# Performance work log

Hardware: AMD Instinct MI355X
Metric: run time of the kernel (lower is better)

The kernel has to match this reference:

```python
import jax, jax.numpy as jnp
import numpy as np

N = 40000          # spots (nodes)
G = 3000           # genes (input features)
C = 20             # num_classes
E = N * 16         # edges (avg degree 16)


def _uniform(key, shape, stdv):
    return jax.random.uniform(key, shape, jnp.float32, -stdv, stdv)


def _linear_params(key, n_in, n_out):
    # torch Linear default init: U(-1/sqrt(in), 1/sqrt(in)); stored as [in, out]
    k1, k2 = jax.random.split(key)
    s = 1.0 / np.sqrt(n_in)
    return _uniform(k1, (n_in, n_out), s), _uniform(k2, (n_out,), s)


def setup_inputs() -> dict:
    key = jax.random.key(0)
    ks = jax.random.split(key, 32)
    x = jax.random.normal(ks[0], (N, G), jnp.float32)
    adj_rows = jax.random.randint(ks[1], (E,), 0, N, jnp.int32)
    adj_cols = jax.random.randint(ks[2], (E,), 0, N, jnp.int32)
    adj_vals = jax.random.uniform(ks[3], (E,), jnp.float32)

    # GCN weights: GraphConvolution init U(-1/sqrt(out), 1/sqrt(out)), no bias
    def gcn_w(k, fi, fo):
        return _uniform(k, (fi, fo), 1.0 / np.sqrt(fo))

    inp = {
        "x": x, "adj_rows": adj_rows, "adj_cols": adj_cols, "adj_vals": adj_vals,
        "W1": gcn_w(ks[4], G, 512), "W2": gcn_w(ks[5], 512, 256),
        "W3": gcn_w(ks[6], 256, 128), "W4": gcn_w(ks[7], 128, 128),
        "W5": gcn_w(ks[8], 128, C),
    }
    # AE linear layers
    for name, (fi, fo), k in [
        ("enc1", (G, 512), ks[9]), ("enc2", (512, 256), ks[10]),
        ("enc3", (256, 128), ks[11]), ("zl", (128, 128), ks[12]),
        ("dec1", (128, 128), ks[13]), ("dec2", (128, 256), ks[14]),
        ("dec3", (256, 512), ks[15]), ("xbar", (512, G), ks[16]),
    ]:
        w, b = _linear_params(k, fi, fo)
        inp[name + "_w"], inp[name + "_b"] = w, b
    # Attention projection vectors (Linear(in_size, 1, bias=False))
    inp["a1"] = _uniform(ks[17], (512,), 1.0 / np.sqrt(512))
    inp["a2"] = _uniform(ks[18], (256,), 1.0 / np.sqrt(256))
    inp["a3"] = _uniform(ks[19], (128,), 1.0 / np.sqrt(128))
    inp["a4"] = _uniform(ks[20], (128,), 1.0 / np.sqrt(128))
    inp["scale"] = jax.random.normal(ks[21], (G,), jnp.float32)
    inp["additive"] = jax.random.normal(ks[22], (G,), jnp.float32)
    return inp


def _spmm(rows, cols, vals, dense, n):
    # out[r] = sum_e vals[e] * dense[cols[e]] for rows[e]==r  (sparse [n,n] @ dense)
    return jax.ops.segment_sum(vals[:, None] * dense[cols], rows, num_segments=n)


def _gcn(x, rows, cols, vals, W, n, active=True):
    out = _spmm(rows, cols, vals, x @ W, n)
    return jax.nn.relu(out) if active else out


def _attn(h, t, a):
    # stack two [N,D] branches, softmax over the branch axis, weighted sum
    z = jnp.stack([h, t], axis=1)           # [N,2,D]
    w = jnp.einsum('nbd,d->nb', z, a)        # [N,2]
    beta = jax.nn.softmax(w, axis=1)
    return jnp.einsum('nb,nbd->nd', beta, z)


def reference(x, adj_rows, adj_cols, adj_vals,
              W1, W2, W3, W4, W5,
              enc1_w, enc1_b, enc2_w, enc2_b, enc3_w, enc3_b, zl_w, zl_b,
              dec1_w, dec1_b, dec2_w, dec2_b, dec3_w, dec3_b, xbar_w, xbar_b,
              a1, a2, a3, a4, scale, additive):
    n = x.shape[0]
    # autoencoder
    t1 = jax.nn.relu(x @ enc1_w + enc1_b)
    t2 = jax.nn.relu(t1 @ enc2_w + enc2_b)
    t3 = jax.nn.relu(t2 @ enc3_w + enc3_b)
    z = t3 @ zl_w + zl_b
    d1 = jax.nn.relu(z @ dec1_w + dec1_b)
    d2 = jax.nn.relu(d1 @ dec2_w + dec2_b)
    d3 = jax.nn.relu(d2 @ dec3_w + dec3_b)
    x_bar = d3 @ xbar_w + xbar_b
    # GCN stack with attention-fused AE skip connections
    h = _gcn(x, adj_rows, adj_cols, adj_vals, W1, n)
    emb = _attn(h, t1, a1)
    h = _gcn(emb, adj_rows, adj_cols, adj_vals, W2, n)
    emb = _attn(h, t2, a2)
    h = _gcn(emb, adj_rows, adj_cols, adj_vals, W3, n)
    emb = _attn(h, t3, a3)
    h = _gcn(emb, adj_rows, adj_cols, adj_vals, W4, n)
    emb = _attn(h, z, a4)
    output = _gcn(emb, adj_rows, adj_cols, adj_vals, W5, n, active=False)
    return output, x_bar, jax.nn.sigmoid(scale), jnp.exp(additive)
```

## Files before the change

### kernel.cpp

```cpp
#include <hip/hip_runtime.h>
#include <cmath>

typedef unsigned short u16;
typedef unsigned int u32;
typedef __attribute__((ext_vector_type(8))) short short8;
typedef __attribute__((ext_vector_type(4))) short short4v;
typedef __attribute__((ext_vector_type(4))) float f32x4;

__device__ __forceinline__ float bf2f(u16 h) {
  union { u32 u; float f; } v; v.u = ((u32)h) << 16; return v.f;
}
__device__ __forceinline__ u16 f2bf(float f) {
  union { float f; u32 u; } v; v.f = f;
  u32 u = v.u;
  u32 r = (u + 0x7FFFu + ((u >> 16) & 1u)) >> 16;
  return (u16)r;
}

__global__ void convx_kernel(const float* __restrict__ x, u16* __restrict__ A0) {
  int idx = blockIdx.x * 256 + threadIdx.x;
  int r = blockIdx.y;
  if (idx >= 752) return;
  short4v o;
  if (r < 40000 && idx < 750) {
    float4 v = *(const float4*)(x + (size_t)r * 3000 + idx * 4);
    o[0] = (short)f2bf(v.x); o[1] = (short)f2bf(v.y);
    o[2] = (short)f2bf(v.z); o[3] = (short)f2bf(v.w);
  } else {
    o[0] = 0; o[1] = 0; o[2] = 0; o[3] = 0;
  }
  *(short4v*)(A0 + (size_t)r * 3008 + idx * 4) = o;
}

__global__ void convw_kernel(const float* __restrict__ W, u16* __restrict__ Wt,
                             int K, int N, int Kp) {
  int k = blockIdx.x * 256 + threadIdx.x;
  int n = blockIdx.y;
  if (k >= Kp) return;
  float v = (k < K && n < N) ? W[(size_t)k * N + n] : 0.f;
  Wt[(size_t)n * Kp + k] = f2bf(v);
}

__global__ void zero_kernel(int* p, int n) {
  int i = blockIdx.x * 256 + threadIdx.x;
  if (i < n) p[i] = 0;
}
__global__ void count_kernel(const int* __restrict__ rows, int* __restrict__ counts, int E) {
  int i = blockIdx.x * 256 + threadIdx.x;
  if (i < E) atomicAdd(&counts[rows[i]], 1);
}
__global__ __launch_bounds__(1024) void scan_kernel(const int* __restrict__ counts,
                                                    int* __restrict__ rowptr,
                                                    int* __restrict__ cursor, int n) {
  __shared__ int buf[1024];
  __shared__ int carry_s;
  int tid = threadIdx.x;
  if (tid == 0) carry_s = 0;
  __syncthreads();
  for (int base = 0; base < n; base += 1024) {
    int i = base + tid;
    int v = (i < n) ? counts[i] : 0;
    buf[tid] = v;
    __syncthreads();
    for (int off = 1; off < 1024; off <<= 1) {
      int tv = (tid >= off) ? buf[tid - off] : 0;
      __syncthreads();
      buf[tid] += tv;
      __syncthreads();
    }
    int incl = buf[tid];
    int carry = carry_s;
    if (i < n) { int ex = carry + incl - v; rowptr[i] = ex; cursor[i] = ex; }
    __syncthreads();
    if (tid == 1023) carry_s = carry + incl;
    __syncthreads();
  }
  if (tid == 0) rowptr[n] = carry_s;
}
__global__ void scatter_kernel(const int* __restrict__ rows, const int* __restrict__ cols,
                               const float* __restrict__ vals, int* __restrict__ cursor,
                               int* __restrict__ cols_s, float* __restrict__ vals_s, int E) {
  int i = blockIdx.x * 256 + threadIdx.x;
  if (i < E) {
    int r = rows[i];
    int p = atomicAdd(&cursor[r], 1);
    cols_s[p] = cols[i];
    vals_s[p] = vals[i];
  }
}

#define BM 128
#define BN 128
#define BK 32

template <bool BIAS, bool RELU, bool OUTBF16, int CH>
__global__ __launch_bounds__(256, 2) void gemm_bf16(
    const u16* __restrict__ A, int lda, const u16* __restrict__ Bt, int ldb,
    void* __restrict__ C1, int ldc,
    const float* __restrict__ bias, int M, int Nreal, int K, int MT, int NT) {
  __shared__ __align__(16) u16 As[2][BM * BK];
  __shared__ __align__(16) u16 Bs[2][BN * BK];
  const int lin = blockIdx.x;
  const int per = CH * NT;
  const int g = lin / per;
  const int r0 = lin - g * per;
  const int bx0 = g * CH;
  const int cw = min(CH, MT - bx0);
  const int bx = bx0 + r0 % cw;
  const int by = r0 / cw;

  const int tid = threadIdx.x;
  const int lane = tid & 63;
  const int wave = tid >> 6;
  const int mblk = bx * BM;
  const int nblk = by * BN;
  const int wm = (wave & 1) * 64;
  const int wn = (wave >> 1) * 64;
  const int ml = lane & 15;
  const int kg = lane >> 4;

  f32x4 acc[4][4];
#pragma unroll
  for (int i = 0; i < 4; ++i)
#pragma unroll
    for (int j = 0; j < 4; ++j) acc[i][j] = (f32x4)(0.f);

  const int nk = K / BK;
  const int sr = tid >> 2;
  const int sc = (tid & 3) * 8;
  const u16* gA0 = A + (size_t)(mblk + sr) * lda + sc;
  const u16* gA1 = A + (size_t)(mblk + sr + 64) * lda + sc;
  const u16* gB0 = Bt + (size_t)(nblk + sr) * ldb + sc;
  const u16* gB1 = Bt + (size_t)(nblk + sr + 64) * ldb + sc;

  auto stage = [&](int buf, int kt) {
    const int ko = kt * BK;
    u16* lA = &As[buf][0] + wave * 512;
    u16* lB = &Bs[buf][0] + wave * 512;
    __builtin_amdgcn_global_load_lds((const void*)(gA0 + ko), (void*)lA, 16, 0, 0);
    __builtin_amdgcn_global_load_lds((const void*)(gA1 + ko), (void*)(lA + 2048), 16, 0, 0);
    __builtin_amdgcn_global_load_lds((const void*)(gB0 + ko), (void*)lB, 16, 0, 0);
    __builtin_amdgcn_global_load_lds((const void*)(gB1 + ko), (void*)(lB + 2048), 16, 0, 0);
  };

  stage(0, 0);
  asm volatile("s_waitcnt vmcnt(0)" ::: "memory");
  __syncthreads();

  int cur = 0;
  for (int kt = 0; kt < nk; ++kt) {
    if (kt + 1 < nk) stage(cur ^ 1, kt + 1);
    short8 af[4], bfr[4];
#pragma unroll
    for (int i = 0; i < 4; ++i) {
      af[i] = *(const short8*)&As[cur][(wm + i * 16 + ml) * BK + kg * 8];
      bfr[i] = *(const short8*)&Bs[cur][(wn + i * 16 + ml) * BK + kg * 8];
    }
#pragma unroll
    for (int i = 0; i < 4; ++i)
#pragma unroll
      for (int j = 0; j < 4; ++j)
        acc[i][j] = __builtin_amdgcn_mfma_f32_16x16x32_bf16(af[i], bfr[j], acc[i][j], 0, 0, 0);
    asm volatile("s_waitcnt vmcnt(0)" ::: "memory");
    __syncthreads();
    cur ^= 1;
  }

#pragma unroll
  for (int i = 0; i < 4; ++i) {
    const int row0 = mblk + wm + i * 16 + kg * 4;
#pragma unroll
    for (int j = 0; j < 4; ++j) {
      const int col = nblk + wn + j * 16 + ml;
      if (col < Nreal) {
        float bv = BIAS ? bias[col] : 0.f;
#pragma unroll
        for (int r = 0; r < 4; ++r) {
          const int row = row0 + r;
          if (row < M) {
            float v = acc[i][j][r] + bv;
            if (RELU) v = fmaxf(v, 0.f);
            if (OUTBF16)
              ((u16*)C1)[(size_t)row * ldc + col] = f2bf(v);
            else
              ((float*)C1)[(size_t)row * ldc + col] = v;
          }
        }
      }
    }
  }
}

template <bool BIAS, bool RELU, bool OUTBF16, bool SPLIT>
__global__ __launch_bounds__(512, 1) void gemm256(
    const u16* __restrict__ A, int lda, const u16* __restrict__ Bt, int ldb,
    void* __restrict__ C1, void* __restrict__ C2, int ldc,
    const float* __restrict__ bias, int M, int Nreal, int K, int MT2, int NT) {
  __shared__ __align__(16) u16 lds[2][2][256 * 64];
  const int tid = threadIdx.x;
  const int lane = tid & 63;
  const int wave = tid >> 6;
  const int wm = wave >> 2;
  const int wn = wave & 3;
  const int ml = lane & 15;
  const int kg = lane >> 4;

  const int grp = blockIdx.x / (8 * NT);
  const int rr = blockIdx.x % (8 * NT);
  const int nb = min(8, MT2 - grp * 8);
  const int bx = grp * 8 + rr % nb;
  const int by = rr / nb;
  const int mblk = bx * 256;
  const int nblk = by * 256;

  f32x4 acc[8][4];
#pragma unroll
  for (int i = 0; i < 8; ++i)
#pragma unroll
    for (int j = 0; j < 4; ++j) acc[i][j] = (f32x4)(0.f);

  const int srow = tid >> 3;
  const int clog = (tid & 7) ^ (srow & 7);
  const size_t abase = (size_t)(mblk + srow) * lda + clog * 8;
  const size_t bbase = (size_t)(nblk + srow) * ldb + clog * 8;
  const int NKT = K / 64;

  auto stageA = [&](int d, int kt, int h) {
    u16* dst = &lds[d][0][0] + h * 4096 + wave * 512;
    const u16* src = A + abase + (size_t)h * 64 * lda + kt * 64;
    __builtin_amdgcn_global_load_lds((const void*)src, (void*)dst, 16, 0, 0);
  };
  auto stageB = [&](int d, int kt, int h) {
    u16* dst = &lds[d][1][0] + h * 4096 + wave * 512;
    const u16* src = Bt + bbase + (size_t)h * 64 * ldb + kt * 64;
    __builtin_amdgcn_global_load_lds((const void*)src, (void*)dst, 16, 0, 0);
  };
  auto stageAll = [&](int d, int kt) {
    stageB(d, kt, 0); stageB(d, kt, 1); stageB(d, kt, 2); stageB(d, kt, 3);
    stageA(d, kt, 0); stageA(d, kt, 2); stageA(d, kt, 1); stageA(d, kt, 3);
  };
  auto readA = [&](int d, int im, int kk) -> short8 {
    const int r = wm * 128 + im * 16 + ml;
    const int ch = (kk * 4 + kg) ^ (r & 7);
    return *(const short8*)&lds[d][0][r * 64 + ch * 8];
  };
  auto readB = [&](int d, int j, int kk) -> short8 {
    const int r = wn * 64 + j * 16 + ml;
    const int ch = (kk * 4 + kg) ^ (r & 7);
    return *(const short8*)&lds[d][1][r * 64 + ch * 8];
  };

  stageAll(0, 0);
  asm volatile("s_waitcnt vmcnt(2)" ::: "memory");
  __builtin_amdgcn_s_barrier();

  for (int kt = 0; kt < NKT; ++kt) {
    const int d = kt & 1;
    const bool more = (kt + 1 < NKT);
    short8 bf2[4][2];
#pragma unroll
    for (int q = 0; q < 4; ++q) {
      if (q == 0) {
        if (more) stageAll(d ^ 1, kt + 1);
#pragma unroll
        for (int j = 0; j < 4; ++j) { bf2[j][0] = readB(d, j, 0); bf2[j][1] = readB(d, j, 1); }
      }
      short8 a00 = readA(d, 2 * q, 0);
      short8 a01 = readA(d, 2 * q, 1);
      short8 a10 = readA(d, 2 * q + 1, 0);
      short8 a11 = readA(d, 2 * q + 1, 1);
      __builtin_amdgcn_s_barrier();
      asm volatile("s_waitcnt lgkmcnt(0)" ::: "memory");
      __builtin_amdgcn_s_setprio(1);
#pragma unroll
      for (int j = 0; j < 4; ++j) {
        acc[2 * q][j]     = __builtin_amdgcn_mfma_f32_16x16x32_bf16(a00, bf2[j][0], acc[2 * q][j], 0, 0, 0);
        acc[2 * q + 1][j] = __builtin_amdgcn_mfma_f32_16x16x32_bf16(a10, bf2[j][0], acc[2 * q + 1][j], 0, 0, 0);
      }
#pragma unroll
      for (int j = 0; j < 4; ++j) {
        acc[2 * q][j]     = __builtin_amdgcn_mfma_f32_16x16x32_bf16(a01, bf2[j][1], acc[2 * q][j], 0, 0, 0);
        acc[2 * q + 1][j] = __builtin_amdgcn_mfma_f32_16x16x32_bf16(a11, bf2[j][1], acc[2 * q + 1][j], 0, 0, 0);
      }
      __builtin_amdgcn_s_setprio(0);
      if (q == 0) {
        if (more) asm volatile("s_waitcnt vmcnt(8)" ::: "memory");
        else      asm volatile("s_waitcnt vmcnt(0)" ::: "memory");
      }
      if (q == 3 && more) asm volatile("s_waitcnt vmcnt(2)" ::: "memory");
      __builtin_amdgcn_s_barrier();
    }
  }

  const int crow0 = mblk + wm * 128;
  const int ccol0 = nblk + wn * 64;
#pragma unroll
  for (int i = 0; i < 8; ++i) {
    const int row0 = crow0 + i * 16 + kg * 4;
#pragma unroll
    for (int j = 0; j < 4; ++j) {
      const int col = ccol0 + j * 16 + ml;
      if (SPLIT) {
        const bool second = (nblk >= 512);
        const float bv = second ? 0.f : bias[col];
#pragma unroll
        for (int r = 0; r < 4; ++r) {
          const int row = row0 + r;
          if (row < M) {
            float v = acc[i][j][r] + bv;
            if (!second) v = fmaxf(v, 0.f);
            u16* dst = second ? (u16*)C2 : (u16*)C1;
            dst[(size_t)row * 512 + (second ? col - 512 : col)] = f2bf(v);
          }
        }
      } else if (col < Nreal) {
        const float bv = BIAS ? bias[col] : 0.f;
#pragma unroll
        for (int r = 0; r < 4; ++r) {
          const int row = row0 + r;
          if (row < M) {
            float v = acc[i][j][r] + bv;
            if (RELU) v = fmaxf(v, 0.f);
            if (OUTBF16)
              ((u16*)C1)[(size_t)row * ldc + col] = f2bf(v);
            else
              ((float*)C1)[(size_t)row * ldc + col] = v;
          }
        }
      }
    }
  }
}

template <int D, bool RELU>
__global__ __launch_bounds__(256) void spmm_vec(const int* __restrict__ rowptr,
                                                const int* __restrict__ colidx,
                                                const float* __restrict__ vals,
                                                const u16* __restrict__ X,
                                                u16* __restrict__ Y) {
  constexpr int VE = D / 64;
  const int wave = threadIdx.x >> 6, lane = threadIdx.x & 63;
  const int row = blockIdx.x * 4 + wave;
  const int co = lane * VE;
  float acc[VE];
#pragma unroll
  for (int j = 0; j < VE; ++j) acc[j] = 0.f;
  const int s = rowptr[row], e = rowptr[row + 1];
  for (int i = s; i < e; ++i) {
    const int c = colidx[i];
    const float v = vals[i];
    const u16* xr = X + (size_t)c * D + co;
    if constexpr (VE == 8) {
      short8 x8 = *(const short8*)xr;
#pragma unroll
      for (int j = 0; j < 8; ++j) acc[j] += v * bf2f((u16)x8[j]);
    } else if constexpr (VE == 4) {
      short4v x4 = *(const short4v*)xr;
#pragma unroll
      for (int j = 0; j < 4; ++j) acc[j] += v * bf2f((u16)x4[j]);
    } else {
      u32 x2 = *(const u32*)xr;
      acc[0] += v * bf2f((u16)(x2 & 0xffffu));
      acc[1] += v * bf2f((u16)(x2 >> 16));
    }
  }
  u16* yr = Y + (size_t)row * D + co;
  if constexpr (VE == 8) {
    short8 o;
#pragma unroll
    for (int j = 0; j < 8; ++j) { float f = RELU ? fmaxf(acc[j], 0.f) : acc[j]; o[j] = (short)f2bf(f); }
    *(short8*)yr = o;
  } else if constexpr (VE == 4) {
    short4v o;
#pragma unroll
    for (int j = 0; j < 4; ++j) { float f = RELU ? fmaxf(acc[j], 0.f) : acc[j]; o[j] = (short)f2bf(f); }
    *(short4v*)yr = o;
  } else {
    float f0 = RELU ? fmaxf(acc[0], 0.f) : acc[0];
    float f1 = RELU ? fmaxf(acc[1], 0.f) : acc[1];
    *(u32*)yr = (u32)f2bf(f0) | ((u32)f2bf(f1) << 16);
  }
}

__global__ __launch_bounds__(64) void spmm_out_kernel(const int* __restrict__ rowptr,
                                                      const int* __restrict__ colidx,
                                                      const float* __restrict__ vals,
                                                      const u16* __restrict__ X,
                                                      float* __restrict__ Y) {
  int row = blockIdx.x;
  int c = threadIdx.x;
  float acc = 0.f;
  int s = rowptr[row], e = rowptr[row + 1];
  for (int i = s; i < e; ++i) {
    int col = colidx[i];
    float v = vals[i];
    if (c < 20) acc += v * bf2f(X[(size_t)col * 20 + c]);
  }
  if (c < 20) Y[(size_t)row * 20 + c] = acc;
}

template <int D>
__global__ __launch_bounds__(256) void attn_vec(const u16* __restrict__ h,
                                                const u16* __restrict__ t,
                                                const float* __restrict__ a,
                                                u16* __restrict__ emb) {
  constexpr int VE = D / 64;
  const int wave = threadIdx.x >> 6, lane = threadIdx.x & 63;
  const int row = blockIdx.x * 4 + wave;
  const int co = lane * VE;
  const u16* hr = h + (size_t)row * D + co;
  const u16* tr = t + (size_t)row * D + co;
  float hv[VE], tv[VE];
  if constexpr (VE == 8) {
    short8 h8 = *(const short8*)hr, t8 = *(const short8*)tr;
#pragma unroll
    for (int j = 0; j < 8; ++j) { hv[j] = bf2f((u16)h8[j]); tv[j] = bf2f((u16)t8[j]); }
  } else if constexpr (VE == 4) {
    short4v h4 = *(const short4v*)hr, t4 = *(const short4v*)tr;
#pragma unroll
    for (int j = 0; j < 4; ++j) { hv[j] = bf2f((u16)h4[j]); tv[j] = bf2f((u16)t4[j]); }
  } else {
    u32 h2 = *(const u32*)hr, t2 = *(const u32*)tr;
    hv[0] = bf2f((u16)(h2 & 0xffffu)); hv[1] = bf2f((u16)(h2 >> 16));
    tv[0] = bf2f((u16)(t2 & 0xffffu)); tv[1] = bf2f((u16)(t2 >> 16));
  }
  float wh = 0.f, wt = 0.f;
#pragma unroll
  for (int j = 0; j < VE; ++j) {
    float av = a[co + j];
    wh += av * hv[j];
    wt += av * tv[j];
  }
  for (int off = 32; off; off >>= 1) {
    wh += __shfl_xor(wh, off);
    wt += __shfl_xor(wt, off);
  }
  float m = fmaxf(wh, wt);
  float e1 = expf(wh - m), e2 = expf(wt - m);
  float inv = 1.f / (e1 + e2);
  float b1 = e1 * inv, b2 = e2 * inv;
  u16* er = emb + (size_t)row * D + co;
  if constexpr (VE == 8) {
    short8 o;
#pragma unroll
    for (int j = 0; j < 8; ++j) o[j] = (short)f2bf(b1 * hv[j] + b2 * tv[j]);
    *(short8*)er = o;
  } else if constexpr (VE == 4) {
    short4v o;
#pragma unroll
    for (int j = 0; j < 4; ++j) o[j] = (short)f2bf(b1 * hv[j] + b2 * tv[j]);
    *(short4v*)er = o;
  } else {
    *(u32*)er = (u32)f2bf(b1 * hv[0] + b2 * tv[0]) | ((u32)f2bf(b1 * hv[1] + b2 * tv[1]) << 16);
  }
}

__global__ __launch_bounds__(64) void xw5_kernel(const u16* __restrict__ emb,
                                                 const float* __restrict__ W5,
                                                 u16* __restrict__ xw5) {
  int row = blockIdx.x;
  int c = threadIdx.x;
  if (c >= 20) return;
  const short8* er = (const short8*)(emb + (size_t)row * 128);
  float acc = 0.f;
#pragma unroll
  for (int k8 = 0; k8 < 16; ++k8) {
    short8 v = er[k8];
#pragma unroll
    for (int j = 0; j < 8; ++j) acc += bf2f((u16)v[j]) * W5[(k8 * 8 + j) * 20 + c];
  }
  xw5[(size_t)row * 20 + c] = f2bf(acc);
}

__global__ void sig_exp_kernel(const float* __restrict__ scale, const float* __restrict__ additive,
                               float* __restrict__ osig, float* __restrict__ oexp, int g) {
  int i = blockIdx.x * 256 + threadIdx.x;
  if (i < g) {
    osig[i] = 1.f / (1.f + expf(-scale[i]));
    oexp[i] = expf(additive[i]);
  }
}

extern "C" void kernel_launch(void* const* d_in, const int* in_sizes, int n_in,
                              void* d_out, int out_size, void* d_ws, size_t ws_size,
                              hipStream_t stream) {
  (void)n_in; (void)out_size; (void)ws_size;
  const float* x      = (const float*)d_in[0];
  const int*   arows  = (const int*)d_in[1];
  const int*   acols  = (const int*)d_in[2];
  const float* avals  = (const float*)d_in[3];
  const float* W1     = (const float*)d_in[4];
  const float* W2     = (const float*)d_in[5];
  const float* W3     = (const float*)d_in[6];
  const float* W4     = (const float*)d_in[7];
  const float* W5     = (const float*)d_in[8];
  const float* enc1_w = (const float*)d_in[9],  *enc1_b = (const float*)d_in[10];
  const float* enc2_w = (const float*)d_in[11], *enc2_b = (const float*)d_in[12];
  const float* enc3_w = (const float*)d_in[13], *enc3_b = (const float*)d_in[14];
  const float* zl_w   = (const float*)d_in[15], *zl_b   = (const float*)d_in[16];
  const float* dec1_w = (const float*)d_in[17], *dec1_b = (const float*)d_in[18];
  const float* dec2_w = (const float*)d_in[19], *dec2_b = (const float*)d_in[20];
  const float* dec3_w = (const float*)d_in[21], *dec3_b = (const float*)d_in[22];
  const float* xbar_w = (const float*)d_in[23], *xbar_b = (const float*)d_in[24];
  const float* a1 = (const float*)d_in[25], *a2 = (const float*)d_in[26];
  const float* a3 = (const float*)d_in[27], *a4 = (const float*)d_in[28];
  const float* scale = (const float*)d_in[29], *additive = (const float*)d_in[30];

  const int E = in_sizes[1];
  const int N = 40000, G = 3000, Kx = 3008;
  const int Mp = 40192;

  float* out      = (float*)d_out;
  float* out_gcn  = out;
  float* out_xbar = out + (size_t)N * 20;
  float* out_sig  = out_xbar + (size_t)N * G;
  float* out_exp  = out_sig + G;

  char* wsb = (char*)d_ws;
  size_t off = 0;
  auto alloc = [&](size_t b) -> void* {
    void* p = wsb + off;
    off = (off + b + 255) & ~(size_t)255;
    return p;
  };
  u16* A0    = (u16*)alloc((size_t)Mp * Kx * 2);
  u16* t1    = (u16*)alloc((size_t)Mp * 512 * 2);
  u16* t2    = (u16*)alloc((size_t)Mp * 256 * 2);
  u16* t3    = (u16*)alloc((size_t)Mp * 128 * 2);
  u16* zb    = (u16*)alloc((size_t)Mp * 128 * 2);
  u16* dd1   = (u16*)alloc((size_t)Mp * 128 * 2);
  u16* dd2   = (u16*)alloc((size_t)Mp * 256 * 2);
  u16* dd3   = (u16*)alloc((size_t)Mp * 512 * 2);
  u16* xw    = (u16*)alloc((size_t)Mp * 512 * 2);
  u16* hb    = (u16*)alloc((size_t)Mp * 512 * 2);
  u16* emb   = (u16*)alloc((size_t)Mp * 512 * 2);
  u16* xw5   = (u16*)alloc((size_t)N * 20 * 2);
  u16* catT  = (u16*)alloc((size_t)1024 * Kx * 2);
  u16* enc2T = (u16*)alloc((size_t)256 * 512 * 2);
  u16* enc3T = (u16*)alloc((size_t)128 * 256 * 2);
  u16* zlT   = (u16*)alloc((size_t)128 * 128 * 2);
  u16* dec1T = (u16*)alloc((size_t)128 * 128 * 2);
  u16* dec2T = (u16*)alloc((size_t)256 * 128 * 2);
  u16* dec3T = (u16*)alloc((size_t)512 * 256 * 2);
  u16* xbarT = (u16*)alloc((size_t)3072 * 512 * 2);
  u16* W2T   = (u16*)alloc((size_t)256 * 512 * 2);
  u16* W3T   = (u16*)alloc((size_t)128 * 256 * 2);
  u16* W4T   = (u16*)alloc((size_t)128 * 128 * 2);
  int* counts = (int*)alloc((size_t)N * 4);
  int* rowptr = (int*)alloc((size_t)(N + 1) * 4);
  int* cursor = (int*)alloc((size_t)N * 4);
  int* colss  = (int*)alloc((size_t)E * 4);
  float* valss = (float*)alloc((size_t)E * 4);

  convx_kernel<<<dim3(3, Mp), 256, 0, stream>>>(x, A0);
  auto convw = [&](const float* W, u16* Wt, int K, int Nw, int Kp, int Np) {
    convw_kernel<<<dim3((Kp + 255) / 256, Np), 256, 0, stream>>>(W, Wt, K, Nw, Kp);
  };
  convw(enc1_w, catT,             3000, 512, Kx, 512);
  convw(W1,     catT + 512 * Kx,  3000, 512, Kx, 512);
  convw(enc2_w, enc2T, 512, 256, 512, 256);
  convw(enc3_w, enc3T, 256, 128, 256, 128);
  convw(zl_w,   zlT,   128, 128, 128, 128);
  convw(dec1_w, dec1T, 128, 128, 128, 128);
  convw(dec2_w, dec2T, 128, 256, 128, 256);
  convw(dec3_w, dec3T, 256, 512, 256, 512);
  convw(xbar_w, xbarT, 512, 3000, 512, 3072);
  convw(W2,     W2T,   512, 256, 512, 256);
  convw(W3,     W3T,   256, 128, 256, 128);
  convw(W4,     W4T,   128, 128, 128, 128);

  zero_kernel<<<(N + 255) / 256, 256, 0, stream>>>(counts, N);
  count_kernel<<<(E + 255) / 256, 256, 0, stream>>>(arows, counts, E);
  scan_kernel<<<1, 1024, 0, stream>>>(counts, rowptr, cursor, N);
  scatter_kernel<<<(E + 255) / 256, 256, 0, stream>>>(arows, acols, avals, cursor, colss, valss, E);

  const int MT = 313;
  const int MT2 = 157;
  gemm256<false, false, true, true><<<MT2 * 4, 512, 0, stream>>>(
      A0, Kx, catT, Kx, t1, xw, 512, enc1_b, N, 1024, Kx, MT2, 4);
  gemm_bf16<true, true, true, 32><<<MT * 2, 256, 0, stream>>>(
      t1, 512, enc2T, 512, t2, 256, enc2_b, N, 256, 512, MT, 2);
  gemm_bf16<true, true, true, 32><<<MT * 1, 256, 0, stream>>>(
      t2, 256, enc3T, 256, t3, 128, enc3_b, N, 128, 256, MT, 1);
  gemm_bf16<true, false, true, 32><<<MT * 1, 256, 0, stream>>>(
      t3, 128, zlT, 128, zb, 128, zl_b, N, 128, 128, MT, 1);
  gemm_bf16<true, true, true, 32><<<MT * 1, 256, 0, stream>>>(
      zb, 128, dec1T, 128, dd1, 128, dec1_b, N, 128, 128, MT, 1);
  gemm_bf16<true, true, true, 32><<<MT * 2, 256, 0, stream>>>(
      dd1, 128, dec2T, 128, dd2, 256, dec2_b, N, 256, 128, MT, 2);
  gemm256<true, true, true, false><<<MT2 * 2, 512, 0, stream>>>(
      dd2, 256, dec3T, 256, dd3, nullptr, 512, dec3_b, N, 512, 256, MT2, 2);
  gemm256<true, false, false, false><<<MT2 * 12, 512, 0, stream>>>(
      dd3, 512, xbarT, 512, out_xbar, nullptr, 3000, xbar_b, N, 3000, 512, MT2, 12);

  spmm_vec<512, true><<<N / 4, 256, 0, stream>>>(rowptr, colss, valss, xw, hb);
  attn_vec<512><<<N / 4, 256, 0, stream>>>(hb, t1, a1, emb);
  gemm_bf16<false, false, true, 32><<<MT * 2, 256, 0, stream>>>(
      emb, 512, W2T, 512, xw, 256, nullptr, N, 256, 512, MT, 2);
  spmm_vec<256, true><<<N / 4, 256, 0, stream>>>(rowptr, colss, valss, xw, hb);
  attn_vec<256><<<N / 4, 256, 0, stream>>>(hb, t2, a2, emb);
  gemm_bf16<false, false, true, 32><<<MT * 1, 256, 0, stream>>>(
      emb, 256, W3T, 256, xw, 128, nullptr, N, 128, 256, MT, 1);
  spmm_vec<128, true><<<N / 4, 256, 0, stream>>>(rowptr, colss, valss, xw, hb);
  attn_vec<128><<<N / 4, 256, 0, stream>>>(hb, t3, a3, emb);
  gemm_bf16<false, false, true, 32><<<MT * 1, 256, 0, stream>>>(
      emb, 128, W4T, 128, xw, 128, nullptr, N, 128, 128, MT, 1);
  spmm_vec<128, true><<<N / 4, 256, 0, stream>>>(rowptr, colss, valss, xw, hb);
  attn_vec<128><<<N / 4, 256, 0, stream>>>(hb, zb, a4, emb);

  xw5_kernel<<<N, 64, 0, stream>>>(emb, W5, xw5);
  spmm_out_kernel<<<N, 64, 0, stream>>>(rowptr, colss, valss, xw5, out_gcn);

  sig_exp_kernel<<<(G + 255) / 256, 256, 0, stream>>>(scale, additive, out_sig, out_exp, G);
}
```

Before: 1.514 ms.

## Replace fine-grained GEMM barrier schedule with register double-buffered A fragments

```diff
diff --git a/kernel.cpp b/kernel.cpp
--- a/kernel.cpp
+++ b/kernel.cpp
@@ -237,7 +237,7 @@
   };
   auto stageAll = [&](int d, int kt) {
     stageB(d, kt, 0); stageB(d, kt, 1); stageB(d, kt, 2); stageB(d, kt, 3);
-    stageA(d, kt, 0); stageA(d, kt, 2); stageA(d, kt, 1); stageA(d, kt, 3);
+    stageA(d, kt, 0); stageA(d, kt, 1); stageA(d, kt, 2); stageA(d, kt, 3);
   };
   auto readA = [&](int d, int im, int kk) -> short8 {
     const int r = wm * 128 + im * 16 + ml;
@@ -251,45 +251,39 @@
   };
 
   stageAll(0, 0);
-  asm volatile("s_waitcnt vmcnt(2)" ::: "memory");
-  __builtin_amdgcn_s_barrier();
+  __syncthreads();
 
   for (int kt = 0; kt < NKT; ++kt) {
     const int d = kt & 1;
-    const bool more = (kt + 1 < NKT);
-    short8 bf2[4][2];
+    if (kt + 1 < NKT) stageAll(d ^ 1, kt + 1);
+
+    short8 b[4][2];
+#pragma unroll
+    for (int j = 0; j < 4; ++j) { b[j][0] = readB(d, j, 0); b[j][1] = readB(d, j, 1); }
+    short8 aC0k0 = readA(d, 0, 0), aC0k1 = readA(d, 0, 1);
+    short8 aC1k0 = readA(d, 1, 0), aC1k1 = readA(d, 1, 1);
 #pragma unroll
     for (int q = 0; q < 4; ++q) {
-      if (q == 0) {
-        if (more) stageAll(d ^ 1, kt + 1);
-#pragma unroll
-        for (int j = 0; j < 4; ++j) { bf2[j][0] = readB(d, j, 0); bf2[j][1] = readB(d, j, 1); }
+      short8 aN0k0, aN0k1, aN1k0, aN1k1;
+      if (q < 3) {
+        aN0k0 = readA(d, 2 * (q + 1), 0);     aN0k1 = readA(d, 2 * (q + 1), 1);
+        aN1k0 = readA(d, 2 * (q + 1) + 1, 0); aN1k1 = readA(d, 2 * (q + 1) + 1, 1);
       }
-      short8 a00 = readA(d, 2 * q, 0);
-      short8 a01 = readA(d, 2 * q, 1);
-      short8 a10 = readA(d, 2 * q + 1, 0);
-      short8 a11 = readA(d, 2 * q + 1, 1);
-      __builtin_amdgcn_s_barrier();
-      asm volatile("s_waitcnt lgkmcnt(0)" ::: "memory");
       __builtin_amdgcn_s_setprio(1);
 #pragma unroll
       for (int j = 0; j < 4; ++j) {
-        acc[2 * q][j]     = __builtin_amdgcn_mfma_f32_16x16x32_bf16(a00, bf2[j][0], acc[2 * q][j], 0, 0, 0);
-        acc[2 * q + 1][j] = __builtin_amdgcn_mfma_f32_16x16x32_bf16(a10, bf2[j][0], acc[2 * q + 1][j], 0, 0, 0);
+        acc[2 * q][j]     = __builtin_amdgcn_mfma_f32_16x16x32_bf16(aC0k0, b[j][0], acc[2 * q][j], 0, 0, 0);
+        acc[2 * q + 1][j] = __builtin_amdgcn_mfma_f32_16x16x32_bf16(aC1k0, b[j][0], acc[2 * q + 1][j], 0, 0, 0);
       }
 #pragma unroll
       for (int j = 0; j < 4; ++j) {
-        acc[2 * q][j]     = __builtin_amdgcn_mfma_f32_16x16x32_bf16(a01, bf2[j][1], acc[2 * q][j], 0, 0, 0);
-        acc[2 * q + 1][j] = __builtin_amdgcn_mfma_f32_16x16x32_bf16(a11, bf2[j][1], acc[2 * q + 1][j], 0, 0, 0);
+        acc[2 * q][j]     = __builtin_amdgcn_mfma_f32_16x16x32_bf16(aC0k1, b[j][1], acc[2 * q][j], 0, 0, 0);
+        acc[2 * q + 1][j] = __builtin_amdgcn_mfma_f32_16x16x32_bf16(aC1k1, b[j][1], acc[2 * q + 1][j], 0, 0, 0);
       }
       __builtin_amdgcn_s_setprio(0);
-      if (q == 0) {
-        if (more) asm volatile("s_waitcnt vmcnt(8)" ::: "memory");
-        else      asm volatile("s_waitcnt vmcnt(0)" ::: "memory");
-      }
-      if (q == 3 && more) asm volatile("s_waitcnt vmcnt(2)" ::: "memory");
-      __builtin_amdgcn_s_barrier();
+      if (q < 3) { aC0k0 = aN0k0; aC0k1 = aN0k1; aC1k0 = aN1k0; aC1k1 = aN1k1; }
     }
+    __syncthreads();
   }
 
   const int crow0 = mblk + wm * 128;
```

Measured after the change: 1.472 ms. 1.03x faster.
